# Kernel optimization log

Hardware: AMD Instinct MI355X
Metric: run time of the kernel (lower is better)

The kernel has to match this reference:

```python
import jax, jax.numpy as jnp
import numpy as np

R = 4          # corr_radius
SLOPE = 0.1    # leaky relu negative slope


def _conv(x, w, b, pad):
    y = jax.lax.conv_general_dilated(
        x, w, window_strides=(1, 1), padding=[(pad, pad), (pad, pad)],
        dimension_numbers=("NCHW", "OIHW", "NCHW"))
    return y + b[None, :, None, None]


def _correlation(x1, x2):
    # Fused windowed cost volume: cv[b, i*(2R+1)+j, h, w] = mean_c x1[b,c,h,w] * x2[b,c,h+i-R,w+j-R]
    B, C, H, W = x1.shape
    x2p = jnp.pad(x2, ((0, 0), (0, 0), (R, R), (R, R)))
    cv = jnp.stack(
        [jnp.mean(x1 * jax.lax.dynamic_slice(x2p, (0, 0, i, j), (B, C, H, W)), axis=1)
         for i in range(2 * R + 1) for j in range(2 * R + 1)], axis=1)
    return cv  # (B, (2R+1)^2, H, W)


def setup_inputs() -> dict:
    key = jax.random.key(0)
    ks = jax.random.split(key, 20)
    B, H, W = 2, 256, 256
    pyr = 24
    inp = {
        "feat0": jax.random.normal(ks[0], (B, 2 * pyr, H, W), jnp.float32),
        "feat1": jax.random.normal(ks[1], (B, 2 * pyr, H, W), jnp.float32),
        "last_feat": jax.random.normal(ks[2], (B, 64, H, W), jnp.float32),
        "last_flow": jax.random.normal(ks[3], (B, 4, H, W), jnp.float32),
    }
    in_ch = (2 * R + 1) ** 2 + 2 * (2 * pyr) + 64 + 4  # 245
    dims = [(160, in_ch, 1), (128, 160, 3), (112, 128, 3), (96, 112, 3), (64, 96, 3), (4, 64, 3)]
    for n, (co, ci, k) in enumerate(dims, 1):
        scale = 1.0 / np.sqrt(ci * k * k)
        inp[f"w{n}"] = jax.random.normal(ks[4 + 2 * n], (co, ci, k, k), jnp.float32) * scale
        inp[f"b{n}"] = jnp.zeros((co,), jnp.float32)
    return inp


def reference(feat0, feat1, last_feat, last_flow,
              w1, b1, w2, b2, w3, b3, w4, b4, w5, b5, w6, b6):
    lrelu = lambda x: jax.nn.leaky_relu(x, SLOPE)
    volume = lrelu(_correlation(feat0, feat1))
    feat = jnp.concatenate([volume, feat0, feat1, last_feat, last_flow], axis=1)
    x = lrelu(_conv(feat, w1, b1, 0))   # 1x1 conv
    x = lrelu(_conv(x, w2, b2, 1))
    x = lrelu(_conv(x, w3, b3, 1))
    x = lrelu(_conv(x, w4, b4, 1))
    x = lrelu(_conv(x, w5, b5, 1))
    flow = _conv(x, w6, b6, 1)          # final ConvBlock, act=None
    return flow, x
```

## Files before the change

kernel.cpp:

```cpp
#include <hip/hip_runtime.h>
#include <hip/hip_fp16.h>
#include <cstdint>
#include <cstddef>


using short8 = __attribute__((ext_vector_type(8))) short;
using f32x4  = __attribute__((ext_vector_type(4))) float;
typedef unsigned short u16;

__device__ __forceinline__ u16 rne_bf16(float f) {
  unsigned u = __float_as_uint(f);
  u += 0x7FFFu + ((u >> 16) & 1u);
  return (u16)(u >> 16);
}

__device__ __forceinline__ void mfma16(const short8& a, const short8& b, f32x4& c) {
  asm("v_mfma_f32_16x16x32_bf16 %0, %1, %2, %0" : "+v"(c) : "v"(a), "v"(b));
}

__device__ __forceinline__ unsigned pk_f16(float a, float b) {
  unsigned r;
  asm("v_cvt_pkrtz_f16_f32 %0, %1, %2" : "=v"(r) : "v"(a), "v"(b));
  return r;
}

__device__ __forceinline__ void dot2(float& acc, unsigned a, unsigned b) {
  asm("v_dot2_f32_f16 %0, %1, %2, %0" : "+v"(acc) : "v"(a), "v"(b));
}

__device__ __forceinline__ void gload16(const void* g, void* l) {
  __builtin_amdgcn_global_load_lds(
      (const __attribute__((address_space(1))) unsigned int*)g,
      (__attribute__((address_space(3))) unsigned int*)l, 16, 0, 0);
}

__device__ __forceinline__ uint2 quad_to_bf16(uint2 v) {
  __half2 lo = *(__half2*)&v.x, hi = *(__half2*)&v.y;
  uint2 u;
  u.x = (unsigned)rne_bf16(__half2float(lo.x)) | ((unsigned)rne_bf16(__half2float(lo.y)) << 16);
  u.y = (unsigned)rne_bf16(__half2float(hi.x)) | ((unsigned)rne_bf16(__half2float(hi.y)) << 16);
  return u;
}

__global__ __launch_bounds__(256) void prep1_kernel(const float* __restrict__ w1,
                                                    u16* __restrict__ w1p) {
  int idx = blockIdx.x * 256 + threadIdx.x;
  int co = idx >> 8, cip = idx & 255;
  float v = 0.f;
  if (co < 160 && cip < 245) {
    int ci = (cip < 164) ? (cip + 81) : (cip - 164);
    v = w1[co * 245 + ci];
  }
  w1p[idx] = rne_bf16(v);
}

template<int CO, int CIr, int BM, int APLN, int CIP>
__global__ __launch_bounds__(256) void prep3s_kernel(const float* __restrict__ w,
                                                     u16* __restrict__ wp) {
  int idx = blockIdx.x * 256 + threadIdx.x;
  int ci = idx % CIP; int rest = idx / CIP;
  int row = rest % APLN; int dyp = rest / APLN;
  int dx = row / BM, co = row % BM;
  float v = 0.f;
  if (dx < 3 && co < CO && ci < CIr)
    v = w[(co * CIr + ci) * 9 + dyp * 3 + dx];
  wp[idx] = rne_bf16(v);
}

template<int CO, int CI, int COP, int CIP>
__global__ __launch_bounds__(256) void prep3_kernel(const float* __restrict__ w,
                                                    u16* __restrict__ wp) {
  int idx = blockIdx.x * 256 + threadIdx.x;
  int ci = idx % CIP; int rest = idx / CIP;
  int co = rest % COP; int tap = rest / COP;
  float v = 0.f;
  if (co < CO && ci < CI) v = w[(co * CI + ci) * 9 + tap];
  wp[idx] = rne_bf16(v);
}

__global__ __launch_bounds__(256) void prep_bias_kernel(const float* __restrict__ b1,
    const float* __restrict__ b2, const float* __restrict__ b3,
    const float* __restrict__ b4, const float* __restrict__ b5,
    float* __restrict__ bp, u16* __restrict__ zbuf) {
  int i = blockIdx.x * 256 + threadIdx.x;
  if (i < 128) zbuf[i] = 0;
  float v = 0.f;
  if (i < 160) v = b1[i];
  else if (i < 288) v = b2[i - 160];
  else if (i < 416) { int c = i - 288; v = (c < 112) ? b3[c] : 0.f; }
  else if (i < 512) v = b4[i - 416];
  else if (i < 576) v = b5[i - 512];
  else return;
  bp[i] = v;
}

__global__ __launch_bounds__(256) void concat_all_kernel(const float* __restrict__ f0,
    const float* __restrict__ f1, const float* __restrict__ lf,
    const float* __restrict__ lfl, u16* __restrict__ X1,
    u16* __restrict__ f0q, u16* __restrict__ f1q) {
  __shared__ float s[16][68];
  const int t = threadIdx.x;
  const size_t px0 = (size_t)blockIdx.x * 64;
  const int b = blockIdx.x >> 10;
  const int hw0 = (blockIdx.x & 1023) * 64;

#pragma unroll 1
  for (int cc = 0; cc < 11; ++cc) {
    __syncthreads();
    {
      int px = t & 63, cg = t >> 6;
#pragma unroll
      for (int r = 0; r < 4; ++r) {
        int cl = cg * 4 + r;
        int c = cc * 16 + cl;
        int hw = hw0 + px;
        float v = 0.f;
        if (c < 48)       v = f0[(((size_t)(b * 48 + c)) << 16) + hw];
        else if (c < 96)  v = f1[(((size_t)(b * 48 + (c - 48))) << 16) + hw];
        else if (c < 160) v = lf[(((size_t)(b * 64 + (c - 96))) << 16) + hw];
        else if (c < 164) v = lfl[(((size_t)(b * 4 + (c - 160))) << 16) + hw];
        s[cl][px] = v;
      }
    }
    __syncthreads();
    {
      int px = t >> 2, g = t & 3;
      int cbase = cc * 16 + g * 4;
      if (cbase < 96) {
        int qq = cbase >> 2;
        u16* dq = (qq < 12) ? (f0q + ((size_t)((b * 12 + qq) << 16) << 2))
                            : (f1q + ((size_t)((b * 12 + qq - 12) << 16) << 2));
        uint2 u;
        u.x = pk_f16(s[g * 4 + 0][px], s[g * 4 + 1][px]);
        u.y = pk_f16(s[g * 4 + 2][px], s[g * 4 + 3][px]);
        *(uint2*)(dq + (size_t)(hw0 + px) * 4) = u;
      } else if (cbase < 164) {
        ushort4 u;
        u.x = rne_bf16(s[g * 4 + 0][px]);
        u.y = rne_bf16(s[g * 4 + 1][px]);
        u.z = rne_bf16(s[g * 4 + 2][px]);
        u.w = rne_bf16(s[g * 4 + 3][px]);
        *(ushort4*)(X1 + (px0 + px) * 256 + cbase) = u;
      }
    }
  }
}

template<int NDY>
__device__ __forceinline__ void corr_acc(const uint2* __restrict__ wb,
                                         const unsigned* __restrict__ f0p,
                                         float* __restrict__ cv,
                                         int row, int col, int dy0) {
#pragma unroll
  for (int d = 0; d < NDY; ++d) {
    const int r = row + dy0 + d;
#pragma unroll
    for (int q = 0; q < 3; ++q) {
      const uint2* base = wb + (q * 10 + r) * 80 + (col + 4);
#pragma unroll
      for (int dx = 0; dx < 9; ++dx) {
        const uint2 v = base[dx];
        dot2(cv[d * 9 + dx], v.x, f0p[2 * q]);
        dot2(cv[d * 9 + dx], v.y, f0p[2 * q + 1]);
      }
    }
  }
}

__global__ __launch_bounds__(256, 4) void corr5_kernel(const u16* __restrict__ f0q,
                                                       const u16* __restrict__ f1q,
                                                       const u16* __restrict__ zbuf,
                                                       u16* __restrict__ X1) {
  __shared__ char wlds[2][20480];
  const int bid = blockIdx.x;
  const int swz = (bid & 7) * 128 + (bid >> 3);
  const int b = swz >> 9, rest = swz & 511;
  const int hp = rest >> 2, ct = rest & 3;
  const int h0 = hp << 1, w0 = ct << 6;
  const int tid = threadIdx.x, lane = tid & 63, wv = tid >> 6;
  const int half = wv >> 1, row = wv & 1, col = lane;
  const int pixhw = ((h0 + row) << 8) + (w0 + col);
  const size_t pix = ((size_t)b << 16) + pixhw;

  const u16* srcp[5];
  bool okf[5];
#pragma unroll
  for (int ru = 0; ru < 5; ++ru) {
    int u = ru * 256 + tid;
    int uq = u / 400;
    int rem = u - uq * 400;
    int r = rem / 40, cu = rem - r * 40;
    int hin = h0 + r - 4;
    int wpx = w0 - 8 + 2 * cu;
    bool ok = (u < 1200) && ((unsigned)hin < 256u) && ((unsigned)wpx < 256u);
    okf[ru] = ok;
    srcp[ru] = ok ? (f1q + (((size_t)((b * 12 + uq) << 16) + (hin << 8) + wpx) << 2))
                  : zbuf;
  }

  float cv[45];
#pragma unroll
  for (int t = 0; t < 45; ++t) cv[t] = 0.f;

#pragma unroll
  for (int ru = 0; ru < 5; ++ru)
    gload16(srcp[ru], &wlds[0][ru * 4096 + wv * 1024]);

#pragma unroll 1
  for (int cc = 0; cc < 4; ++cc) {
    __syncthreads();
    if (cc < 3) {
#pragma unroll
      for (int ru = 0; ru < 5; ++ru) {
        const u16* s = okf[ru] ? (srcp[ru] + (size_t)(cc + 1) * 786432) : zbuf;
        gload16(s, &wlds[(cc + 1) & 1][ru * 4096 + wv * 1024]);
      }
    }
    const uint2* wb = (const uint2*)&wlds[cc & 1][0];

    const u16* f0base = f0q + (((size_t)((b * 12 + cc * 3) << 16) + pixhw) << 2);
    uint2 q0 = *(const uint2*)(f0base);
    uint2 q1 = *(const uint2*)(f0base + 262144);
    uint2 q2 = *(const uint2*)(f0base + 524288);
    unsigned f0p[6] = {q0.x, q0.y, q1.x, q1.y, q2.x, q2.y};

    {
      u16* dst0 = X1 + pix * 256 + cc * 12;
      *(uint2*)(dst0)     = quad_to_bf16(q0);
      *(uint2*)(dst0 + 4) = quad_to_bf16(q1);
      *(uint2*)(dst0 + 8) = quad_to_bf16(q2);
    }
    {
      u16* dst1 = X1 + pix * 256 + 48 + cc * 12;
#pragma unroll
      for (int q = 0; q < 3; ++q) {
        uint2 v = wb[(q * 10 + row + 4) * 80 + (col + 8)];
        *(uint2*)(dst1 + 4 * q) = quad_to_bf16(v);
      }
    }
    if (half == 0) corr_acc<4>(wb, f0p, cv, row, col, 0);
    else           corr_acc<5>(wb, f0p, cv, row, col, 4);
  }

  u16* dst = X1 + pix * 256;
  const float sc = 1.0f / 48.0f;
  if (half == 0) {
#pragma unroll
    for (int qq = 0; qq < 9; ++qq) {
      u16 e[4];
#pragma unroll
      for (int j = 0; j < 4; ++j) {
        float v = cv[qq * 4 + j] * sc;
        v = v > 0.f ? v : 0.1f * v;
        e[j] = rne_bf16(v);
      }
      uint2 u;
      u.x = (unsigned)e[0] | ((unsigned)e[1] << 16);
      u.y = (unsigned)e[2] | ((unsigned)e[3] << 16);
      *(uint2*)(dst + 164 + qq * 4) = u;
    }
  } else {
#pragma unroll
    for (int qq = 0; qq < 14; ++qq) {
      u16 e[4];
#pragma unroll
      for (int j = 0; j < 4; ++j) {
        int t = qq * 4 + j;
        float v = 0.f;
        if (t < 45) {
          v = cv[t] * sc;
          v = v > 0.f ? v : 0.1f * v;
        }
        e[j] = rne_bf16(v);
      }
      uint2 u;
      u.x = (unsigned)e[0] | ((unsigned)e[1] << 16);
      u.y = (unsigned)e[2] | ((unsigned)e[3] << 16);
      *(uint2*)(dst + 200 + qq * 4) = u;
    }
  }
}

template<int CI, int BM, int APLN, int KS, int OSTRIDE, bool LRELU, bool OBF, int COF32>
__global__ __launch_bounds__(256) void convs_kernel(const u16* __restrict__ Xin,
    const u16* __restrict__ Wp, const float* __restrict__ bias,
    const u16* __restrict__ zbuf, u16* __restrict__ Xout,
    float* __restrict__ outF) {
  constexpr int NCH = CI / 32;
  constexpr int NDX = (KS == 3) ? 3 : 1;
  constexpr int AROUNDS = APLN / 64;
  constexpr int BROUNDS = (KS == 3) ? 3 : 2;
  constexpr int MF = BM / 32;
  constexpr int AELEMS = AROUNDS * 2048;
  constexpr int BPXMAX = (KS == 3) ? 132 : 128;
  __shared__ u16 lds[(AROUNDS + BROUNDS) * 2048];

  const int tid = threadIdx.x;
  const int lane = tid & 63, wv = tid >> 6;
  const int wm = wv >> 1, wn = wv & 1;
  const int bid = blockIdx.x;
  const int swz = (bid & 7) * 128 + (bid >> 3);
  const int bi = swz >> 9;
  const int h = (swz >> 1) & 255;
  const int w0 = (swz & 1) << 7;
  const int l15 = lane & 15, segr = lane >> 4;

  size_t aofs[AROUNDS];
#pragma unroll
  for (int r = 0; r < AROUNDS; ++r) {
    int slot = r * 256 + tid;
    int row = slot >> 2, sp = slot & 3;
    int seg = sp ^ ((row >> 1) & 3);
    aofs[r] = (size_t)row * CI + seg * 8;
  }
  size_t bofs[BROUNDS];
  bool bcolv[BROUNDS];
#pragma unroll
  for (int r = 0; r < BROUNDS; ++r) {
    int slot = r * 256 + tid;
    int pxl = slot >> 2, sp = slot & 3;
    int seg = sp ^ ((pxl >> 1) & 3);
    int px = (KS == 3) ? (w0 + pxl - 2) : (w0 + pxl);
    bcolv[r] = ((unsigned)px < 256u) && (pxl < BPXMAX);
    bofs[r] = (size_t)px * CI + seg * 8;
  }

  f32x4 acc[MF][4];
  const f32x4 zf = {0.f, 0.f, 0.f, 0.f};
#pragma unroll
  for (int m = 0; m < MF; ++m)
#pragma unroll
    for (int n = 0; n < 4; ++n) acc[m][n] = zf;

  int dy = 0, c = 0;
#pragma unroll 1
  for (int ph = 0; ph < NDX * NCH; ++ph) {
    __syncthreads();
    const u16* Wph = Wp + ((size_t)dy * APLN) * CI + c * 32;
#pragma unroll
    for (int r = 0; r < AROUNDS; ++r)
      gload16(Wph + aofs[r], &lds[r * 2048 + wv * 512]);
    const int hin = (KS == 3) ? (h + dy - 1) : h;
    const bool rv = (unsigned)hin < 256u;
    const u16* Brow = Xin + ((size_t)((bi << 8) + (rv ? hin : 0)) << 8) * CI + c * 32;
#pragma unroll
    for (int r = 0; r < BROUNDS; ++r) {
      const u16* src = (rv && bcolv[r]) ? (Brow + bofs[r]) : zbuf;
      gload16(src, &lds[AELEMS + r * 2048 + wv * 512]);
    }
    __syncthreads();

#pragma unroll
    for (int dx = 0; dx < NDX; ++dx) {
      short8 bfr[4];
#pragma unroll
      for (int n = 0; n < 4; ++n) {
        int p = wn * 64 + n * 16 + l15;
        int pxl = (KS == 3) ? (p + dx + 1) : p;
        int ba = (AELEMS * 2) + pxl * 64 + ((segr ^ ((pxl >> 1) & 3)) << 4);
        bfr[n] = *(const short8*)((const char*)lds + ba);
      }
      short8 afr[MF];
#pragma unroll
      for (int m = 0; m < MF; ++m) {
        int row = dx * BM + wm * (BM / 2) + m * 16 + l15;
        int aa = row * 64 + ((segr ^ ((row >> 1) & 3)) << 4);
        afr[m] = *(const short8*)((const char*)lds + aa);
      }
#pragma unroll
      for (int m = 0; m < MF; ++m)
#pragma unroll
        for (int n = 0; n < 4; ++n) mfma16(afr[m], bfr[n], acc[m][n]);
    }
    if (++c == NCH) { c = 0; ++dy; }
  }
  asm volatile("s_nop 7\n\ts_nop 7");

  const int co_sub = (lane >> 4) << 2;
  const size_t pixbase = ((size_t)((bi << 8) + h)) << 8;
#pragma unroll
  for (int m = 0; m < MF; ++m) {
    const int co = wm * (BM / 2) + m * 16 + co_sub;
#pragma unroll
    for (int n = 0; n < 4; ++n) {
      const int px = w0 + wn * 64 + n * 16 + l15;
      f32x4 v = acc[m][n];
      float t[4];
#pragma unroll
      for (int r = 0; r < 4; ++r) {
        float x = v[r] + bias[co + r];
        if (LRELU) x = x > 0.f ? x : 0.1f * x;
        t[r] = x;
      }
      if (OBF) {
        ushort4 u;
        u.x = rne_bf16(t[0]); u.y = rne_bf16(t[1]);
        u.z = rne_bf16(t[2]); u.w = rne_bf16(t[3]);
        *(ushort4*)(Xout + (pixbase + px) * OSTRIDE + co) = u;
      }
      if (COF32 > 0) {
#pragma unroll
        for (int r = 0; r < 4; ++r) {
          int cch = co + r;
          if (cch < COF32)
            outF[(((size_t)bi * COF32 + cch) << 16) + (h << 8) + px] = t[r];
        }
      }
    }
  }
}

template<int CI, int COP, int MF, int KS, bool LRELU, bool OBF, int COF32>
__global__ __launch_bounds__(256) void conv_kernel(const u16* __restrict__ Xin,
                                                   const u16* __restrict__ Wp,
                                                   const float* __restrict__ bias,
                                                   u16* __restrict__ Xout, int ostride,
                                                   float* __restrict__ outF) {
  const int lane = threadIdx.x & 63, wv = threadIdx.x >> 6;
  const int bi = blockIdx.x >> 9;
  const int h = (blockIdx.x >> 1) & 255;
  const int w0 = (blockIdx.x & 1) << 7;
  const int co0 = blockIdx.y * (MF * 16);
  const int l15 = lane & 15, klane = (lane >> 4) << 3;
  const int ncol0 = w0 + wv * 32 + l15;
  const int rowbase = (bi << 8) + h;

  const f32x4 zf = {0.f, 0.f, 0.f, 0.f};
  const short8 z8 = {0, 0, 0, 0, 0, 0, 0, 0};
  f32x4 acc[MF][2];
#pragma unroll
  for (int m = 0; m < MF; ++m) { acc[m][0] = zf; acc[m][1] = zf; }

#pragma unroll 1
  for (int chunk = 0; chunk < CI / 32; ++chunk) {
#pragma unroll
    for (int tap = 0; tap < KS * KS; ++tap) {
      const int dy = (KS == 3) ? tap / 3 - 1 : 0;
      const int dx = (KS == 3) ? tap % 3 - 1 : 0;
      const int hin = h + dy;
      if (KS == 3 && (unsigned)hin >= 256u) continue;
      short8 bf[2];
#pragma unroll
      for (int nf = 0; nf < 2; ++nf) {
        int win = ncol0 + nf * 16 + dx;
        short8 v = z8;
        if (KS == 1 || (unsigned)win < 256u)
          v = *(const short8*)(Xin + ((size_t)(((bi << 8) + hin) * 256 + win)) * CI
                               + chunk * 32 + klane);
        bf[nf] = v;
      }
#pragma unroll
      for (int m = 0; m < MF; ++m) {
        const short8 af = *(const short8*)(Wp + ((size_t)(tap * COP + co0 + m * 16 + l15)) * CI
                                           + chunk * 32 + klane);
        mfma16(af, bf[0], acc[m][0]);
        mfma16(af, bf[1], acc[m][1]);
      }
    }
  }
  asm volatile("s_nop 7\n\ts_nop 7");

  const int co_sub = (lane >> 4) << 2;
  const size_t pixrow = (size_t)rowbase << 8;
#pragma unroll
  for (int m = 0; m < MF; ++m) {
    const int co = co0 + m * 16 + co_sub;
#pragma unroll
    for (int nf = 0; nf < 2; ++nf) {
      const int w = ncol0 + nf * 16;
      f32x4 v = acc[m][nf];
      if constexpr (OBF) {
        float t[4];
#pragma unroll
        for (int r = 0; r < 4; ++r) {
          float x = v[r] + bias[co + r];
          if constexpr (LRELU) x = x > 0.f ? x : 0.1f * x;
          t[r] = x;
        }
        ushort4 u;
        u.x = rne_bf16(t[0]); u.y = rne_bf16(t[1]);
        u.z = rne_bf16(t[2]); u.w = rne_bf16(t[3]);
        *(ushort4*)(Xout + (pixrow + w) * (size_t)ostride + co) = u;
      }
      if constexpr (COF32 > 0) {
#pragma unroll
        for (int r = 0; r < 4; ++r) {
          int c = co + r;
          if (c < COF32) {
            float x = v[r] + bias[c];
            if constexpr (LRELU) x = x > 0.f ? x : 0.1f * x;
            outF[((((size_t)bi * COF32) + c) << 16) + (h << 8) + w] = x;
          }
        }
      }
    }
  }
}

extern "C" void kernel_launch(void* const* d_in, const int* in_sizes, int n_in,
                              void* d_out, int out_size, void* d_ws, size_t ws_size,
                              hipStream_t stream) {
  const float* feat0 = (const float*)d_in[0];
  const float* feat1 = (const float*)d_in[1];
  const float* lfeat = (const float*)d_in[2];
  const float* lflow = (const float*)d_in[3];
  const float* w1 = (const float*)d_in[4];  const float* b1 = (const float*)d_in[5];
  const float* w2 = (const float*)d_in[6];  const float* b2 = (const float*)d_in[7];
  const float* w3 = (const float*)d_in[8];  const float* b3 = (const float*)d_in[9];
  const float* w4 = (const float*)d_in[10]; const float* b4 = (const float*)d_in[11];
  const float* w5 = (const float*)d_in[12]; const float* b5 = (const float*)d_in[13];
  const float* w6 = (const float*)d_in[14]; const float* b6 = (const float*)d_in[15];

  u16* ws = (u16*)d_ws;
  u16* X1 = ws;
  u16* X2 = ws + 33554432;
  u16* X3 = ws;
  u16* X4 = ws + 33554432;
  u16* X5 = ws;
  u16* X6 = ws + 33554432;
  u16* f0q = ws + 33554432;
  u16* f1q = ws + 39845888;
  u16* w1p = ws + 54525952;
  u16* w2p = w1p + 49152;
  u16* w3p = w2p + 184320;
  u16* w4p = w3p + 147456;
  u16* w5p = w4p + 147456;
  u16* w6p = w5p + 55296;
  float* bp = (float*)(w6p + 9216);
  u16* zbuf = (u16*)(bp + 576);

  const float* bp1 = bp;
  const float* bp2 = bp + 160;
  const float* bp3 = bp + 288;
  const float* bp4 = bp + 416;
  const float* bp5 = bp + 512;

  float* flow = (float*)d_out;
  float* xout = (float*)d_out + 524288;

  prep1_kernel<<<192, 256, 0, stream>>>(w1, w1p);
  prep3s_kernel<128, 160, 128, 384, 160><<<720, 256, 0, stream>>>(w2, w2p);
  prep3s_kernel<112, 128, 128, 384, 128><<<576, 256, 0, stream>>>(w3, w3p);
  prep3s_kernel< 96, 112,  96, 320, 128><<<480, 256, 0, stream>>>(w4, w4p);
  prep3s_kernel< 64,  96,  64, 192,  96><<<216, 256, 0, stream>>>(w5, w5p);
  prep3_kernel<  4,  64,  16,  64><<< 36, 256, 0, stream>>>(w6, w6p);
  prep_bias_kernel<<<3, 256, 0, stream>>>(b1, b2, b3, b4, b5, bp, zbuf);

  concat_all_kernel<<<2048, 256, 0, stream>>>(feat0, feat1, lfeat, lflow, X1, f0q, f1q);
  corr5_kernel<<<1024, 256, 0, stream>>>(f0q, f1q, zbuf, X1);

  convs_kernel<256, 160, 192, 1, 160, true, true,  0><<<1024, 256, 0, stream>>>(X1, w1p, bp1, zbuf, X2, nullptr);
  convs_kernel<160, 128, 384, 3, 128, true, true,  0><<<1024, 256, 0, stream>>>(X2, w2p, bp2, zbuf, X3, nullptr);
  convs_kernel<128, 128, 384, 3, 128, true, true,  0><<<1024, 256, 0, stream>>>(X3, w3p, bp3, zbuf, X4, nullptr);
  convs_kernel<128,  96, 320, 3,  96, true, true,  0><<<1024, 256, 0, stream>>>(X4, w4p, bp4, zbuf, X5, nullptr);
  convs_kernel< 96,  64, 192, 3,  64, true, true, 64><<<1024, 256, 0, stream>>>(X5, w5p, bp5, zbuf, X6, xout);
  conv_kernel< 64,  16, 1, 3, false, false, 4><<<dim3(1024, 1), 256, 0, stream>>>(X6, w6p, b6, nullptr, 0, flow);
}
```

Baseline: 312.8 us.

## Double-buffer LDS staging in conv kernel to overlap global loads with MFMA

The conv kernel's K-loop now uses two LDS buffers and issues the global-to-LDS loads for the next phase before computing on the current one. It waits on vmcnt for only the older batch of loads, then hits a barrier. The MFMA section also runs at raised wave priority. This is meant to hide global load latency that the old load-then-sync-then-compute loop left exposed, at the cost of doubling LDS use, which may lower occupancy. The wait_vm helper falls back to vmcnt(0) for any LOADS count it does not list, so some template instances may get no overlap.

```diff
diff --git a/kernel.cpp b/kernel.cpp
--- a/kernel.cpp
+++ b/kernel.cpp
@@ -32,6 +32,15 @@
   __builtin_amdgcn_global_load_lds(
       (const __attribute__((address_space(1))) unsigned int*)g,
       (__attribute__((address_space(3))) unsigned int*)l, 16, 0, 0);
+}
+
+template<int N> __device__ __forceinline__ void wait_vm() {
+  if constexpr (N == 0)      asm volatile("s_waitcnt vmcnt(0)" ::: "memory");
+  else if constexpr (N == 5) asm volatile("s_waitcnt vmcnt(5)" ::: "memory");
+  else if constexpr (N == 6) asm volatile("s_waitcnt vmcnt(6)" ::: "memory");
+  else if constexpr (N == 8) asm volatile("s_waitcnt vmcnt(8)" ::: "memory");
+  else if constexpr (N == 9) asm volatile("s_waitcnt vmcnt(9)" ::: "memory");
+  else                       asm volatile("s_waitcnt vmcnt(0)" ::: "memory");
 }
 
 __device__ __forceinline__ uint2 quad_to_bf16(uint2 v) {
@@ -293,7 +302,9 @@
   constexpr int MF = BM / 32;
   constexpr int AELEMS = AROUNDS * 2048;
   constexpr int BPXMAX = (KS == 3) ? 132 : 128;
-  __shared__ u16 lds[(AROUNDS + BROUNDS) * 2048];
+  constexpr int LOADS = AROUNDS + BROUNDS;
+  constexpr int NPH = NDX * NCH;
+  __shared__ u16 lds[2][LOADS * 2048];
 
   const int tid = threadIdx.x;
   const int lane = tid & 63, wv = tid >> 6;
@@ -325,6 +336,23 @@
     bofs[r] = (size_t)px * CI + seg * 8;
   }
 
+  auto stage = [&](int ph2, int bsel) {
+    const int dy2 = ph2 / NCH;
+    const int c2 = ph2 - dy2 * NCH;
+    const u16* Wph = Wp + ((size_t)dy2 * APLN) * CI + c2 * 32;
+#pragma unroll
+    for (int r = 0; r < AROUNDS; ++r)
+      gload16(Wph + aofs[r], &lds[bsel][r * 2048 + wv * 512]);
+    const int hin = (KS == 3) ? (h + dy2 - 1) : h;
+    const bool rv = (unsigned)hin < 256u;
+    const u16* Brow = Xin + ((size_t)((bi << 8) + (rv ? hin : 0)) << 8) * CI + c2 * 32;
+#pragma unroll
+    for (int r = 0; r < BROUNDS; ++r) {
+      const u16* src = (rv && bcolv[r]) ? (Brow + bofs[r]) : zbuf;
+      gload16(src, &lds[bsel][AELEMS + r * 2048 + wv * 512]);
+    }
+  };
+
   f32x4 acc[MF][4];
   const f32x4 zf = {0.f, 0.f, 0.f, 0.f};
 #pragma unroll
@@ -332,24 +360,23 @@
 #pragma unroll
     for (int n = 0; n < 4; ++n) acc[m][n] = zf;
 
-  int dy = 0, c = 0;
+  stage(0, 0);
+
 #pragma unroll 1
-  for (int ph = 0; ph < NDX * NCH; ++ph) {
-    __syncthreads();
-    const u16* Wph = Wp + ((size_t)dy * APLN) * CI + c * 32;
-#pragma unroll
-    for (int r = 0; r < AROUNDS; ++r)
-      gload16(Wph + aofs[r], &lds[r * 2048 + wv * 512]);
-    const int hin = (KS == 3) ? (h + dy - 1) : h;
-    const bool rv = (unsigned)hin < 256u;
-    const u16* Brow = Xin + ((size_t)((bi << 8) + (rv ? hin : 0)) << 8) * CI + c * 32;
-#pragma unroll
-    for (int r = 0; r < BROUNDS; ++r) {
-      const u16* src = (rv && bcolv[r]) ? (Brow + bofs[r]) : zbuf;
-      gload16(src, &lds[AELEMS + r * 2048 + wv * 512]);
-    }
-    __syncthreads();
-
+  for (int ph = 0; ph < NPH; ++ph) {
+    const int buf = ph & 1;
+    const int dy = (KS == 3) ? (ph / NCH) : 0;
+    if (ph + 1 < NPH) {
+      stage(ph + 1, buf ^ 1);
+      __builtin_amdgcn_sched_barrier(0);
+      wait_vm<LOADS>();
+    } else {
+      wait_vm<0>();
+    }
+    __builtin_amdgcn_s_barrier();
+    __builtin_amdgcn_sched_barrier(0);
+
+    __builtin_amdgcn_s_setprio(1);
 #pragma unroll
     for (int dx = 0; dx < NDX; ++dx) {
       short8 bfr[4];
@@ -357,22 +384,25 @@
       for (int n = 0; n < 4; ++n) {
         int p = wn * 64 + n * 16 + l15;
         int pxl = (KS == 3) ? (p + dx + 1) : p;
-        int ba = (AELEMS * 2) + pxl * 64 + ((segr ^ ((pxl >> 1) & 3)) << 4);
-        bfr[n] = *(const short8*)((const char*)lds + ba);
+        int ba = pxl * 64 + ((segr ^ ((pxl >> 1) & 3)) << 4);
+        bfr[n] = *(const short8*)((const char*)&lds[buf][AELEMS] + ba);
       }
       short8 afr[MF];
 #pragma unroll
       for (int m = 0; m < MF; ++m) {
         int row = dx * BM + wm * (BM / 2) + m * 16 + l15;
         int aa = row * 64 + ((segr ^ ((row >> 1) & 3)) << 4);
-        afr[m] = *(const short8*)((const char*)lds + aa);
+        afr[m] = *(const short8*)((const char*)&lds[buf][0] + aa);
       }
 #pragma unroll
       for (int m = 0; m < MF; ++m)
 #pragma unroll
         for (int n = 0; n < 4; ++n) mfma16(afr[m], bfr[n], acc[m][n]);
     }
-    if (++c == NCH) { c = 0; ++dy; }
+    __builtin_amdgcn_s_setprio(0);
+    asm volatile("s_waitcnt lgkmcnt(0)" ::: "memory");
+    __builtin_amdgcn_sched_barrier(0);
+    __builtin_amdgcn_s_barrier();
   }
   asm volatile("s_nop 7\n\ts_nop 7");
 
```

Measured after the change: 307.1 us. About the same (-1.8%).
